# Performance work log

Measured on AMD Instinct MI355X. Metric: run time of the kernel, lower is better.

Reference implementation:

```python
import jax, jax.numpy as jnp
import numpy as np
from jax.ops import segment_sum

N_NODES = 100000
N_EDGES = 3200000
IN_DIM = 128
HID = 128
INT_DIM = 512
OUT_DIM = 3


def gcn_conv(x, W, b, src, dst, n):
    # PyG GCNConv (eval): add self-loops, symmetric normalization, aggregate, bias.
    loop = jnp.arange(n, dtype=src.dtype)
    s = jnp.concatenate([src, loop])
    d = jnp.concatenate([dst, loop])
    deg = segment_sum(jnp.ones_like(d, dtype=x.dtype), d, num_segments=n)  # [N]
    dinv = jnp.where(deg > 0, jax.lax.rsqrt(jnp.maximum(deg, 1e-12)), 0.0)
    norm = dinv[s] * dinv[d]                      # [E+N]
    h = x @ W                                      # [N, F_out]
    msg = h[s] * norm[:, None]                    # gather + scale
    return segment_sum(msg, d, num_segments=n) + b


def setup_inputs() -> dict:
    key = jax.random.key(0)
    ks = jax.random.split(key, 12)
    def lin(kw, kb, fi, fo):
        lim = 1.0 / np.sqrt(fi)
        W = jax.random.uniform(kw, (fi, fo), jnp.float32, -lim, lim)
        b = jax.random.uniform(kb, (fo,), jnp.float32, -lim, lim)
        return W, b
    x = jax.random.normal(ks[0], (N_NODES, IN_DIM), jnp.float32)
    edge_index = jax.random.randint(ks[1], (2, N_EDGES), 0, N_NODES, dtype=jnp.int64)
    W1, b1 = lin(ks[2], ks[3], IN_DIM, HID)
    W2, b2 = lin(ks[4], ks[5], HID, HID)
    W3, b3 = lin(ks[6], ks[7], HID, INT_DIM)
    Wi, bi = lin(ks[8], ks[9], INT_DIM, INT_DIM)
    Wc, bc = lin(ks[10], ks[11], INT_DIM, OUT_DIM)
    return {"x": x, "edge_index": edge_index, "W1": W1, "b1": b1, "W2": W2,
            "b2": b2, "W3": W3, "b3": b3, "Wi": Wi, "bi": bi, "Wc": Wc, "bc": bc}


def reference(x, edge_index, W1, b1, W2, b2, W3, b3, Wi, bi, Wc, bc):
    src, dst = edge_index[0], edge_index[1]
    n = x.shape[0]
    h = jax.nn.relu(gcn_conv(x, W1, b1, src, dst, n))
    h = jax.nn.relu(gcn_conv(h, W2, b2, src, dst, n))
    h = jax.nn.relu(gcn_conv(h, W3, b3, src, dst, n))
    h = jax.nn.relu(h @ Wi + bi)
    return h @ Wc + bc
```

## Files before the change

### kernel.cpp

```cpp
#include <hip/hip_runtime.h>
#include <hip/hip_fp16.h>

#define NN 100000
#define NE 3200000
#define NB 391
#define NBLK 512
#define EPB 6250

typedef unsigned int uint32;
typedef unsigned short u16;
typedef long long ll64;
typedef __attribute__((ext_vector_type(8))) _Float16 half8;
typedef __attribute__((ext_vector_type(4))) float f32x4;

__device__ inline float2 h2f2(uint32 u) {
  __half2 h = *reinterpret_cast<__half2*>(&u);
  return __half22float2(h);
}
__device__ inline uint32 f2h2(float x, float y) {
  return (uint32)__half_as_ushort(__float2half(x)) |
         ((uint32)__half_as_ushort(__float2half(y)) << 16);
}
__device__ inline int edge_at(const void* ei, int is64, ll64 idx) {
  return is64 ? (int)((const ll64*)ei)[idx] : ((const int*)ei)[idx];
}
__device__ inline int detect64(const int* ei32) {
  int acc = 0;
#pragma unroll
  for (int k = 1; k < 32; k += 2) acc |= ei32[k];
  return (acc == 0) ? 1 : 0;
}

__global__ __launch_bounds__(256) void k_binB(const void* __restrict__ ei,
                                              int* __restrict__ tbl) {
  __shared__ int h[NB];
  __shared__ int sIs64;
  int k = blockIdx.x, tid = threadIdx.x;
  for (int i = tid; i < NB; i += 256) h[i] = 0;
  if (tid == 0) sIs64 = detect64((const int*)ei);
  __syncthreads();
  int is64 = sIs64;
  ll64 beg = (ll64)k * EPB, end = beg + EPB;
  for (ll64 i = beg + tid; i < end; i += 256)
    atomicAdd(&h[edge_at(ei, is64, (ll64)NE + i) >> 8], 1);
  __syncthreads();
  for (int i = tid; i < NB; i += 256) tbl[k * NB + i] = h[i];
}
__global__ __launch_bounds__(512) void k_binC1(int* __restrict__ tbl,
                                               int* __restrict__ total) {
  __shared__ int sd[NBLK];
  int b = blockIdx.x, tid = threadIdx.x;
  int v = tbl[tid * NB + b];
  sd[tid] = v;
  __syncthreads();
  for (int off = 1; off < NBLK; off <<= 1) {
    int t = (tid >= off) ? sd[tid - off] : 0;
    __syncthreads();
    sd[tid] += t;
    __syncthreads();
  }
  tbl[tid * NB + b] = sd[tid] - v;
  if (tid == NBLK - 1) total[b] = sd[NBLK - 1];
}
__global__ __launch_bounds__(512) void k_binC2(const int* __restrict__ total,
                                               int* __restrict__ bbase,
                                               int* __restrict__ offs) {
  __shared__ int sd[512];
  int tid = threadIdx.x;
  int v = (tid < NB) ? total[tid] : 0;
  sd[tid] = v;
  __syncthreads();
  for (int off = 1; off < 512; off <<= 1) {
    int t = (tid >= off) ? sd[tid - off] : 0;
    __syncthreads();
    sd[tid] += t;
    __syncthreads();
  }
  if (tid < NB) bbase[tid] = sd[tid] - v;
  if (tid == 0) offs[NN] = NE;
}
__global__ __launch_bounds__(256) void k_binD(const void* __restrict__ ei,
                                              const int* __restrict__ tbl,
                                              const int* __restrict__ bbase,
                                              uint32* __restrict__ binned) {
  __shared__ int lb[NB];
  __shared__ int lc[NB];
  __shared__ int sIs64;
  int k = blockIdx.x, tid = threadIdx.x;
  for (int i = tid; i < NB; i += 256) {
    lb[i] = tbl[k * NB + i] + bbase[i];
    lc[i] = 0;
  }
  if (tid == 0) sIs64 = detect64((const int*)ei);
  __syncthreads();
  int is64 = sIs64;
  ll64 beg = (ll64)k * EPB, end = beg + EPB;
  for (ll64 i = beg + tid; i < end; i += 256) {
    int s = edge_at(ei, is64, i);
    int d = edge_at(ei, is64, (ll64)NE + i);
    int b = d >> 8;
    int r = atomicAdd(&lc[b], 1);
    binned[lb[b] + r] = (uint32)s | ((uint32)(d & 255) << 24);
  }
}
__global__ __launch_bounds__(256) void k_binE(const uint32* __restrict__ binned,
                                              const int* __restrict__ bbase,
                                              const int* __restrict__ total,
                                              int* __restrict__ offs,
                                              float* __restrict__ dinv,
                                              int* __restrict__ csr) {
  __shared__ int cnt[256], pref[256], fil[256];
  int b = blockIdx.x, tid = threadIdx.x;
  cnt[tid] = 0;
  fil[tid] = 0;
  __syncthreads();
  int base = bbase[b], tot = total[b];
  for (int i = tid; i < tot; i += 256) atomicAdd(&cnt[binned[base + i] >> 24], 1);
  __syncthreads();
  int v = cnt[tid];
  pref[tid] = v;
  __syncthreads();
  for (int off = 1; off < 256; off <<= 1) {
    int t = (tid >= off) ? pref[tid - off] : 0;
    __syncthreads();
    pref[tid] += t;
    __syncthreads();
  }
  int myoff = pref[tid] - v;
  pref[tid] = myoff;
  int node = b * 256 + tid;
  if (node < NN) {
    offs[node] = base + myoff;
    dinv[node] = rsqrtf((float)(v + 1));
  }
  __syncthreads();
  for (int i = tid; i < tot; i += 256) {
    uint32 w = binned[base + i];
    int dl = w >> 24;
    int r = atomicAdd(&fil[dl], 1);
    csr[base + pref[dl] + r] = (int)(w & 0xFFFFFFu);
  }
}

__device__ inline void packOne(const float* __restrict__ W, u16* __restrict__ ph,
                               int K, int N, int t) {
  int j = t & 7, lane = (t >> 3) & 63, tl = t >> 9;
  int kbn = K >> 5;
  int kb = tl % kbn, ntile = tl / kbn;
  int k = kb * 32 + (lane >> 4) * 8 + j;
  int n2 = ntile * 16 + (lane & 15);
  ph[t] = __half_as_ushort(__float2half(W[k * N + n2]));
}
__global__ void k_packhalf(const float* W1, const float* W2, const float* W3,
                           const float* Wi, u16* p1, u16* p2, u16* p3, u16* pi,
                           const float4* __restrict__ x, ushort4* __restrict__ xh,
                           const float* __restrict__ dinv) {
  int t = blockIdx.x * blockDim.x + threadIdx.x;
  if (t < 16384) packOne(W1, p1, 128, 128, t);
  else if (t < 32768) packOne(W2, p2, 128, 128, t - 16384);
  else if (t < 98304) packOne(W3, p3, 128, 512, t - 32768);
  else if (t < 360448) packOne(Wi, pi, 512, 512, t - 98304);
  else {
    int i = t - 360448;
    if (i < NN * 32) {
      float4 v = x[i];
      float sc = dinv[i >> 5];
      ushort4 o;
      o.x = __half_as_ushort(__float2half(v.x * sc));
      o.y = __half_as_ushort(__float2half(v.y * sc));
      o.z = __half_as_ushort(__float2half(v.z * sc));
      o.w = __half_as_ushort(__float2half(v.w * sc));
      xh[i] = o;
    }
  }
}

__global__ void k_agg(const uint32* __restrict__ xi, uint32* __restrict__ o,
                      const int* __restrict__ csr, const int* __restrict__ offs,
                      const float* __restrict__ dinv, int n) {
  int tid = threadIdx.x;
  int lane = tid & 63;
  int sub = lane >> 4, fl = lane & 15;
  int node = blockIdx.x * 16 + (tid >> 6) * 4 + sub;
  if (node >= n) return;
  int beg = offs[node], end = offs[node + 1];
  const uint4* xv = (const uint4*)xi;
  float acc[8] = {};
  int j = beg;
  for (; j + 7 < end; j += 8) {
    int s[8];
    uint4 r[8];
#pragma unroll
    for (int q = 0; q < 8; q++) s[q] = csr[j + q];
#pragma unroll
    for (int q = 0; q < 8; q++) r[q] = xv[(ll64)s[q] * 16 + fl];
#pragma unroll
    for (int q = 0; q < 8; q++) {
      float2 p0 = h2f2(r[q].x), p1 = h2f2(r[q].y);
      float2 p2 = h2f2(r[q].z), p3 = h2f2(r[q].w);
      acc[0] += p0.x; acc[1] += p0.y; acc[2] += p1.x; acc[3] += p1.y;
      acc[4] += p2.x; acc[5] += p2.y; acc[6] += p3.x; acc[7] += p3.y;
    }
  }
  for (; j + 3 < end; j += 4) {
    int s[4];
    uint4 r[4];
#pragma unroll
    for (int q = 0; q < 4; q++) s[q] = csr[j + q];
#pragma unroll
    for (int q = 0; q < 4; q++) r[q] = xv[(ll64)s[q] * 16 + fl];
#pragma unroll
    for (int q = 0; q < 4; q++) {
      float2 p0 = h2f2(r[q].x), p1 = h2f2(r[q].y);
      float2 p2 = h2f2(r[q].z), p3 = h2f2(r[q].w);
      acc[0] += p0.x; acc[1] += p0.y; acc[2] += p1.x; acc[3] += p1.y;
      acc[4] += p2.x; acc[5] += p2.y; acc[6] += p3.x; acc[7] += p3.y;
    }
  }
  for (; j < end; j++) {
    uint4 r = xv[(ll64)csr[j] * 16 + fl];
    float2 p0 = h2f2(r.x), p1 = h2f2(r.y), p2 = h2f2(r.z), p3 = h2f2(r.w);
    acc[0] += p0.x; acc[1] += p0.y; acc[2] += p1.x; acc[3] += p1.y;
    acc[4] += p2.x; acc[5] += p2.y; acc[6] += p3.x; acc[7] += p3.y;
  }
  float di = dinv[node];
  uint4 sf = xv[(ll64)node * 16 + fl];
  float2 q0 = h2f2(sf.x), q1 = h2f2(sf.y), q2 = h2f2(sf.z), q3 = h2f2(sf.w);
  uint4 ov;
  ov.x = f2h2(di * (acc[0] + q0.x), di * (acc[1] + q0.y));
  ov.y = f2h2(di * (acc[2] + q1.x), di * (acc[3] + q1.y));
  ov.z = f2h2(di * (acc[4] + q2.x), di * (acc[5] + q2.y));
  ov.w = f2h2(di * (acc[6] + q3.x), di * (acc[7] + q3.y));
  ((uint4*)o)[(ll64)node * 16 + fl] = ov;
}

__global__ __launch_bounds__(256, 4) void k_gemm_mfma(
    const u16* __restrict__ A, const u16* __restrict__ Bp,
    const float* __restrict__ bias, const float* __restrict__ dscale,
    u16* __restrict__ Co, int M, int N, int K) {
  int wave = threadIdx.x >> 6, lane = threadIdx.x & 63;
  int quad = lane >> 4, l16 = lane & 15;
  int row0 = blockIdx.x * 64, col0 = blockIdx.y * 64;
  int m = row0 + wave * 16 + l16;
  int mc = (m < M) ? m : (M - 1);
  int kbn = K >> 5;
  f32x4 acc[4] = {{0,0,0,0},{0,0,0,0},{0,0,0,0},{0,0,0,0}};
  const half8* Ar = (const half8*)&A[(ll64)mc * K];
  half8 ac = Ar[quad];
  half8 an = ac;
  half8 bc_[4], bn_[4];
#pragma unroll
  for (int nt = 0; nt < 4; nt++)
    bc_[nt] = *(const half8*)&Bp[((ll64)(((col0 >> 4) + nt) * kbn) * 64 + lane) * 8];
  for (int kb = 0; kb < kbn; kb++) {
    int kn = kb + 1;
    if (kn < kbn) {
      an = Ar[kn * 4 + quad];
#pragma unroll
      for (int nt = 0; nt < 4; nt++)
        bn_[nt] = *(const half8*)&Bp[((ll64)(((col0 >> 4) + nt) * kbn + kn) * 64 + lane) * 8];
    }
#pragma unroll
    for (int nt = 0; nt < 4; nt++)
      acc[nt] = __builtin_amdgcn_mfma_f32_16x16x32_f16(ac, bc_[nt], acc[nt], 0, 0, 0);
    ac = an;
#pragma unroll
    for (int nt = 0; nt < 4; nt++) bc_[nt] = bn_[nt];
  }
  float ds[4];
#pragma unroll
  for (int r = 0; r < 4; r++) {
    int rr = row0 + wave * 16 + quad * 4 + r;
    ds[r] = dscale[(rr < M) ? rr : (M - 1)];
  }
#pragma unroll
  for (int nt = 0; nt < 4; nt++) {
    int cc = col0 + nt * 16 + l16;
    float bv = bias[cc];
#pragma unroll
    for (int r = 0; r < 4; r++) {
      int rr = row0 + wave * 16 + quad * 4 + r;
      if (rr < M)
        Co[(ll64)rr * N + cc] =
            __half_as_ushort(__float2half(fmaxf(acc[nt][r] + bv, 0.0f) * ds[r]));
    }
  }
}

__global__ __launch_bounds__(256, 4) void k_tail32(
    const u16* __restrict__ a3, const u16* __restrict__ W3p,
    const float* __restrict__ b3, const u16* __restrict__ Wip,
    const float* __restrict__ bi, const float* __restrict__ Wc,
    const float* __restrict__ bc, float* __restrict__ out, int M) {
  __shared__ u16 h3s[32 * 512];
  __shared__ float sRed[4][32][3];
  int tid = threadIdx.x;
  int wave = tid >> 6, lane = tid & 63, quad = lane >> 4, l16 = lane & 15;
  int row0 = blockIdx.x * 32;

  half8 af[2][4];
#pragma unroll
  for (int rt = 0; rt < 2; rt++) {
    const half8* Ar = (const half8*)&a3[(ll64)(row0 + rt * 16 + l16) * 128];
#pragma unroll
    for (int kb = 0; kb < 4; kb++) af[rt][kb] = Ar[kb * 4 + quad];
  }
  {
    f32x4 acc0 = {0, 0, 0, 0}, acc1 = {0, 0, 0, 0};
    half8 bq[4];
#pragma unroll
    for (int p = 0; p < 3; p++)
      bq[p] = *(const half8*)&W3p[((ll64)(wave * 32 + p) * 64 + lane) * 8];
#pragma unroll 4
    for (int t = 0; t < 32; t++) {
      if (t + 3 < 32)
        bq[(t + 3) & 3] = *(const half8*)&W3p[((ll64)(wave * 32 + t + 3) * 64 + lane) * 8];
      half8 bcur = bq[t & 3];
      int kb = t & 3;
      acc0 = __builtin_amdgcn_mfma_f32_16x16x32_f16(af[0][kb], bcur, acc0, 0, 0, 0);
      acc1 = __builtin_amdgcn_mfma_f32_16x16x32_f16(af[1][kb], bcur, acc1, 0, 0, 0);
      if (kb == 3) {
        int nt = wave * 8 + (t >> 2);
        int col = nt * 16 + l16;
        float bv = b3[col];
#pragma unroll
        for (int r = 0; r < 4; r++) {
          int row0l = quad * 4 + r;
          float v0 = fmaxf(acc0[r] + bv, 0.0f);
          float v1 = fmaxf(acc1[r] + bv, 0.0f);
          int oct0 = (col >> 3) ^ (row0l & 7);
          h3s[row0l * 512 + oct0 * 8 + (col & 7)] = __half_as_ushort(__float2half(v0));
          int row1l = 16 + row0l;
          int oct1 = (col >> 3) ^ (row1l & 7);
          h3s[row1l * 512 + oct1 * 8 + (col & 7)] = __half_as_ushort(__float2half(v1));
        }
        acc0 = (f32x4){0, 0, 0, 0};
        acc1 = (f32x4){0, 0, 0, 0};
      }
    }
  }
  __syncthreads();

  float acc3[2][4][3] = {};
  {
    f32x4 acc0 = {0, 0, 0, 0}, acc1 = {0, 0, 0, 0};
    half8 bq[4];
#pragma unroll
    for (int p = 0; p < 3; p++)
      bq[p] = *(const half8*)&Wip[((ll64)(wave * 128 + p) * 64 + lane) * 8];
    int r0l = l16, r1l = 16 + l16;
    int sw0 = r0l & 7;
#pragma unroll 4
    for (int t = 0; t < 128; t++) {
      if (t + 3 < 128)
        bq[(t + 3) & 3] = *(const half8*)&Wip[((ll64)(wave * 128 + t + 3) * 64 + lane) * 8];
      half8 bcur = bq[t & 3];
      int kb = t & 15;
      int oct = ((kb * 4 + quad) ^ sw0);
      half8 a0 = *(const half8*)&h3s[r0l * 512 + oct * 8];
      half8 a1 = *(const half8*)&h3s[r1l * 512 + oct * 8];
      acc0 = __builtin_amdgcn_mfma_f32_16x16x32_f16(a0, bcur, acc0, 0, 0, 0);
      acc1 = __builtin_amdgcn_mfma_f32_16x16x32_f16(a1, bcur, acc1, 0, 0, 0);
      if (kb == 15) {
        int nt = wave * 8 + (t >> 4);
        int col = nt * 16 + l16;
        float bv = bi[col];
        float w0 = Wc[col * 3 + 0], w1 = Wc[col * 3 + 1], w2 = Wc[col * 3 + 2];
#pragma unroll
        for (int r = 0; r < 4; r++) {
          float v0 = fmaxf(acc0[r] + bv, 0.0f);
          float v1 = fmaxf(acc1[r] + bv, 0.0f);
          acc3[0][r][0] += v0 * w0; acc3[0][r][1] += v0 * w1; acc3[0][r][2] += v0 * w2;
          acc3[1][r][0] += v1 * w0; acc3[1][r][1] += v1 * w1; acc3[1][r][2] += v1 * w2;
        }
        acc0 = (f32x4){0, 0, 0, 0};
        acc1 = (f32x4){0, 0, 0, 0};
      }
    }
  }
#pragma unroll
  for (int rt = 0; rt < 2; rt++)
#pragma unroll
    for (int r = 0; r < 4; r++)
#pragma unroll
      for (int c = 0; c < 3; c++) {
        float v = acc3[rt][r][c];
        v += __shfl_xor(v, 1);
        v += __shfl_xor(v, 2);
        v += __shfl_xor(v, 4);
        v += __shfl_xor(v, 8);
        acc3[rt][r][c] = v;
      }
  if (l16 == 0) {
#pragma unroll
    for (int rt = 0; rt < 2; rt++)
#pragma unroll
      for (int r = 0; r < 4; r++)
#pragma unroll
        for (int c = 0; c < 3; c++)
          sRed[wave][rt * 16 + quad * 4 + r][c] = acc3[rt][r][c];
  }
  __syncthreads();
  if (tid < 96) {
    int row = tid / 3, c = tid % 3;
    out[(ll64)(row0 + row) * 3 + c] = sRed[0][row][c] + sRed[1][row][c] +
                                      sRed[2][row][c] + sRed[3][row][c] + bc[c];
  }
}

extern "C" void kernel_launch(void* const* d_in, const int* in_sizes, int n_in,
                              void* d_out, int out_size, void* d_ws, size_t ws_size,
                              hipStream_t stream) {
  const float* x  = (const float*)d_in[0];
  const void*  ei = d_in[1];
  const float* W1 = (const float*)d_in[2];
  const float* b1 = (const float*)d_in[3];
  const float* W2 = (const float*)d_in[4];
  const float* b2 = (const float*)d_in[5];
  const float* W3 = (const float*)d_in[6];
  const float* b3 = (const float*)d_in[7];
  const float* Wi = (const float*)d_in[8];
  const float* bi = (const float*)d_in[9];
  const float* Wc = (const float*)d_in[10];
  const float* bc = (const float*)d_in[11];
  float* out = (float*)d_out;

  char* ws = (char*)d_ws;
  const ll64 KB = 1ll << 10, MB = 1ll << 20;
  float* dinv  = (float*)(ws + 0);
  int*   offs  = (int*)(ws + 512 * KB);
  int*   total = (int*)(ws + 1 * MB + 64 * KB);
  int*   bbase = (int*)(ws + 1 * MB + 128 * KB);
  int*   tbl   = (int*)(ws + 1 * MB + 192 * KB);
  uint32* binned = (uint32*)(ws + 2 * MB);
  int*   csr   = (int*)(ws + 15 * MB);
  u16* pW1 = (u16*)(ws + 28 * MB);
  u16* pW2 = (u16*)(ws + 28 * MB + 64 * KB);
  u16* pW3 = (u16*)(ws + 28 * MB + 128 * KB);
  u16* pWi = (u16*)(ws + 28 * MB + 512 * KB);
  u16* xh   = (u16*)(ws + 29 * MB);
  u16* bufA = (u16*)(ws + 55 * MB);
  u16* bufB = (u16*)(ws + 81 * MB);

  const int TB = 256;
  k_binB<<<NBLK, TB, 0, stream>>>(ei, tbl);
  k_binC1<<<NB, NBLK, 0, stream>>>(tbl, total);
  k_binC2<<<1, 512, 0, stream>>>(total, bbase, offs);
  k_binD<<<NBLK, TB, 0, stream>>>(ei, tbl, bbase, binned);
  k_binE<<<NB, TB, 0, stream>>>(binned, bbase, total, offs, dinv, csr);
  k_packhalf<<<(360448 + NN * 32 + TB - 1) / TB, TB, 0, stream>>>(
      W1, W2, W3, Wi, pW1, pW2, pW3, pWi, (const float4*)x, (ushort4*)xh, dinv);

  const int MBk = (NN + 63) / 64;
  int aggBlocks = (NN + 15) / 16;
  dim3 g128(MBk, 2);

  k_agg<<<aggBlocks, TB, 0, stream>>>((const uint32*)xh, (uint32*)bufA, csr, offs, dinv, NN);
  k_gemm_mfma<<<g128, TB, 0, stream>>>(bufA, pW1, b1, dinv, bufB, NN, 128, 128);
  k_agg<<<aggBlocks, TB, 0, stream>>>((const uint32*)bufB, (uint32*)bufA, csr, offs, dinv, NN);
  k_gemm_mfma<<<g128, TB, 0, stream>>>(bufA, pW2, b2, dinv, bufB, NN, 128, 128);
  k_agg<<<aggBlocks, TB, 0, stream>>>((const uint32*)bufB, (uint32*)bufA, csr, offs, dinv, NN);
  k_tail32<<<NN / 32, TB, 0, stream>>>(bufA, pW3, b3, pWi, bi, Wc, bc, out, NN);
}
```

Measured before the change: 699.7 us.

## Store aggregation inputs feature-chunk-major so each gather pass hits a cache-sized slice

The aggregation input features are stored in a chunk-major layout: 8 chunks of 16 halfs, each holding all nodes contiguously. Both the x packing kernel and the GEMM epilogue now write that layout. Each aggregation block handles one chunk for 128 nodes, so random source gathers touch only a 3.2MB slice per chunk, which can stay resident in L2/LLC. CSR index loads and output stores become nontemporal. In exchange, the CSR index stream is read 8 times and each gather fetches only 32 bytes per edge.

Result: slower. 1.059 ms (+51.4%).

```diff
diff --git a/kernel.cpp b/kernel.cpp
--- a/kernel.cpp
+++ b/kernel.cpp
@@ -12,6 +12,7 @@
 typedef long long ll64;
 typedef __attribute__((ext_vector_type(8))) _Float16 half8;
 typedef __attribute__((ext_vector_type(4))) float f32x4;
+typedef __attribute__((ext_vector_type(4))) uint32 nt4;
 
 __device__ inline float2 h2f2(uint32 u) {
   __half2 h = *reinterpret_cast<__half2*>(&u);
@@ -170,7 +171,8 @@
       o.y = __half_as_ushort(__float2half(v.y * sc));
       o.z = __half_as_ushort(__float2half(v.z * sc));
       o.w = __half_as_ushort(__float2half(v.w * sc));
-      xh[i] = o;
+      int row = i >> 5, j = i & 31;
+      xh[(ll64)(j >> 2) * (NN * 4) + row * 4 + (j & 3)] = o;
     }
   }
 }
@@ -179,21 +181,25 @@
                       const int* __restrict__ csr, const int* __restrict__ offs,
                       const float* __restrict__ dinv, int n) {
   int tid = threadIdx.x;
+  int chunk = blockIdx.x & 7;
+  int nb = blockIdx.x >> 3;
   int lane = tid & 63;
-  int sub = lane >> 4, fl = lane & 15;
-  int node = blockIdx.x * 16 + (tid >> 6) * 4 + sub;
+  int sub = lane & 1;
+  int nloc = lane >> 1;
+  int node = nb * 128 + (tid >> 6) * 32 + nloc;
   if (node >= n) return;
   int beg = offs[node], end = offs[node + 1];
-  const uint4* xv = (const uint4*)xi;
+  const nt4* xv = (const nt4*)xi;
+  ll64 cbase = (ll64)chunk * (NN * 2);
   float acc[8] = {};
   int j = beg;
   for (; j + 7 < end; j += 8) {
     int s[8];
-    uint4 r[8];
-#pragma unroll
-    for (int q = 0; q < 8; q++) s[q] = csr[j + q];
-#pragma unroll
-    for (int q = 0; q < 8; q++) r[q] = xv[(ll64)s[q] * 16 + fl];
+    nt4 r[8];
+#pragma unroll
+    for (int q = 0; q < 8; q++) s[q] = __builtin_nontemporal_load(&csr[j + q]);
+#pragma unroll
+    for (int q = 0; q < 8; q++) r[q] = xv[cbase + (ll64)s[q] * 2 + sub];
 #pragma unroll
     for (int q = 0; q < 8; q++) {
       float2 p0 = h2f2(r[q].x), p1 = h2f2(r[q].y);
@@ -204,11 +210,11 @@
   }
   for (; j + 3 < end; j += 4) {
     int s[4];
-    uint4 r[4];
-#pragma unroll
-    for (int q = 0; q < 4; q++) s[q] = csr[j + q];
-#pragma unroll
-    for (int q = 0; q < 4; q++) r[q] = xv[(ll64)s[q] * 16 + fl];
+    nt4 r[4];
+#pragma unroll
+    for (int q = 0; q < 4; q++) s[q] = __builtin_nontemporal_load(&csr[j + q]);
+#pragma unroll
+    for (int q = 0; q < 4; q++) r[q] = xv[cbase + (ll64)s[q] * 2 + sub];
 #pragma unroll
     for (int q = 0; q < 4; q++) {
       float2 p0 = h2f2(r[q].x), p1 = h2f2(r[q].y);
@@ -218,20 +224,21 @@
     }
   }
   for (; j < end; j++) {
-    uint4 r = xv[(ll64)csr[j] * 16 + fl];
+    int s = __builtin_nontemporal_load(&csr[j]);
+    nt4 r = xv[cbase + (ll64)s * 2 + sub];
     float2 p0 = h2f2(r.x), p1 = h2f2(r.y), p2 = h2f2(r.z), p3 = h2f2(r.w);
     acc[0] += p0.x; acc[1] += p0.y; acc[2] += p1.x; acc[3] += p1.y;
     acc[4] += p2.x; acc[5] += p2.y; acc[6] += p3.x; acc[7] += p3.y;
   }
   float di = dinv[node];
-  uint4 sf = xv[(ll64)node * 16 + fl];
+  nt4 sf = xv[cbase + (ll64)node * 2 + sub];
   float2 q0 = h2f2(sf.x), q1 = h2f2(sf.y), q2 = h2f2(sf.z), q3 = h2f2(sf.w);
-  uint4 ov;
+  nt4 ov;
   ov.x = f2h2(di * (acc[0] + q0.x), di * (acc[1] + q0.y));
   ov.y = f2h2(di * (acc[2] + q1.x), di * (acc[3] + q1.y));
   ov.z = f2h2(di * (acc[4] + q2.x), di * (acc[5] + q2.y));
   ov.w = f2h2(di * (acc[6] + q3.x), di * (acc[7] + q3.y));
-  ((uint4*)o)[(ll64)node * 16 + fl] = ov;
+  __builtin_nontemporal_store(ov, &((nt4*)o)[(ll64)node * 16 + chunk * 2 + sub]);
 }
 
 __global__ __launch_bounds__(256, 4) void k_gemm_mfma(
@@ -277,11 +284,12 @@
   for (int nt = 0; nt < 4; nt++) {
     int cc = col0 + nt * 16 + l16;
     float bv = bias[cc];
+    ll64 cmaj = (ll64)(cc >> 4) * ((ll64)M * 16);
 #pragma unroll
     for (int r = 0; r < 4; r++) {
       int rr = row0 + wave * 16 + quad * 4 + r;
       if (rr < M)
-        Co[(ll64)rr * N + cc] =
+        Co[cmaj + (ll64)rr * 16 + l16] =
             __half_as_ushort(__float2half(fmaxf(acc[nt][r] + bv, 0.0f) * ds[r]));
     }
   }
@@ -452,7 +460,7 @@
       W1, W2, W3, Wi, pW1, pW2, pW3, pWi, (const float4*)x, (ushort4*)xh, dinv);
 
   const int MBk = (NN + 63) / 64;
-  int aggBlocks = (NN + 15) / 16;
+  int aggBlocks = 8 * ((NN + 127) / 128);
   dim3 g128(MBk, 2);
 
   k_agg<<<aggBlocks, TB, 0, stream>>>((const uint32*)xh, (uint32*)bufA, csr, offs, dinv, NN);
```

## Fuse third-layer aggregation into tail kernel via shared-memory staging

Applied to the files above, without the earlier changes.

The final sparse aggregation now runs inside the tail kernel instead of as a separate k_agg launch. Each block gathers neighbor rows for its 32 nodes, applies the self-loop and dinv scaling, and writes the fp16 result into an XOR-swizzled shared buffer. The MFMA A fragments are then read from that buffer rather than from global memory. This drops one kernel launch and a full write and read of the intermediate activation. The cost is lower gather parallelism per block (4 nodes per wave at a time) and extra synchronisation inside a kernel with heavy register and LDS use.

Result: no change. 690.1 us (-1.4%).

```diff
diff --git a/kernel.cpp b/kernel.cpp
--- a/kernel.cpp
+++ b/kernel.cpp
@@ -287,24 +287,87 @@
   }
 }
 
-__global__ __launch_bounds__(256, 4) void k_tail32(
-    const u16* __restrict__ a3, const u16* __restrict__ W3p,
-    const float* __restrict__ b3, const u16* __restrict__ Wip,
-    const float* __restrict__ bi, const float* __restrict__ Wc,
-    const float* __restrict__ bc, float* __restrict__ out, int M) {
+__global__ __launch_bounds__(256, 4) void k_tail32f(
+    const u16* __restrict__ xin, const int* __restrict__ csr,
+    const int* __restrict__ offs, const float* __restrict__ dinv,
+    const u16* __restrict__ W3p, const float* __restrict__ b3,
+    const u16* __restrict__ Wip, const float* __restrict__ bi,
+    const float* __restrict__ Wc, const float* __restrict__ bc,
+    float* __restrict__ out, int M) {
   __shared__ u16 h3s[32 * 512];
   __shared__ float sRed[4][32][3];
   int tid = threadIdx.x;
   int wave = tid >> 6, lane = tid & 63, quad = lane >> 4, l16 = lane & 15;
   int row0 = blockIdx.x * 32;
 
+  {
+    int sub = lane >> 4, fl = lane & 15;
+    const uint4* xv = (const uint4*)xin;
+#pragma unroll
+    for (int rnd = 0; rnd < 2; rnd++) {
+      int nloc = rnd * 16 + wave * 4 + sub;
+      int node = row0 + nloc;
+      int beg = offs[node], end = offs[node + 1];
+      float acc[8] = {};
+      int j = beg;
+      for (; j + 7 < end; j += 8) {
+        int s[8];
+        uint4 r[8];
+#pragma unroll
+        for (int q = 0; q < 8; q++) s[q] = csr[j + q];
+#pragma unroll
+        for (int q = 0; q < 8; q++) r[q] = xv[(ll64)s[q] * 16 + fl];
+#pragma unroll
+        for (int q = 0; q < 8; q++) {
+          float2 p0 = h2f2(r[q].x), p1 = h2f2(r[q].y);
+          float2 p2 = h2f2(r[q].z), p3 = h2f2(r[q].w);
+          acc[0] += p0.x; acc[1] += p0.y; acc[2] += p1.x; acc[3] += p1.y;
+          acc[4] += p2.x; acc[5] += p2.y; acc[6] += p3.x; acc[7] += p3.y;
+        }
+      }
+      for (; j + 3 < end; j += 4) {
+        int s[4];
+        uint4 r[4];
+#pragma unroll
+        for (int q = 0; q < 4; q++) s[q] = csr[j + q];
+#pragma unroll
+        for (int q = 0; q < 4; q++) r[q] = xv[(ll64)s[q] * 16 + fl];
+#pragma unroll
+        for (int q = 0; q < 4; q++) {
+          float2 p0 = h2f2(r[q].x), p1 = h2f2(r[q].y);
+          float2 p2 = h2f2(r[q].z), p3 = h2f2(r[q].w);
+          acc[0] += p0.x; acc[1] += p0.y; acc[2] += p1.x; acc[3] += p1.y;
+          acc[4] += p2.x; acc[5] += p2.y; acc[6] += p3.x; acc[7] += p3.y;
+        }
+      }
+      for (; j < end; j++) {
+        uint4 r = xv[(ll64)csr[j] * 16 + fl];
+        float2 p0 = h2f2(r.x), p1 = h2f2(r.y), p2 = h2f2(r.z), p3 = h2f2(r.w);
+        acc[0] += p0.x; acc[1] += p0.y; acc[2] += p1.x; acc[3] += p1.y;
+        acc[4] += p2.x; acc[5] += p2.y; acc[6] += p3.x; acc[7] += p3.y;
+      }
+      float di = dinv[node];
+      uint4 sf = xv[(ll64)node * 16 + fl];
+      float2 q0 = h2f2(sf.x), q1 = h2f2(sf.y), q2 = h2f2(sf.z), q3 = h2f2(sf.w);
+      uint4 ov;
+      ov.x = f2h2(di * (acc[0] + q0.x), di * (acc[1] + q0.y));
+      ov.y = f2h2(di * (acc[2] + q1.x), di * (acc[3] + q1.y));
+      ov.z = f2h2(di * (acc[4] + q2.x), di * (acc[5] + q2.y));
+      ov.w = f2h2(di * (acc[6] + q3.x), di * (acc[7] + q3.y));
+      *(uint4*)&h3s[nloc * 128 + ((fl ^ (nloc & 7)) << 3)] = ov;
+    }
+  }
+  __syncthreads();
   half8 af[2][4];
 #pragma unroll
   for (int rt = 0; rt < 2; rt++) {
-    const half8* Ar = (const half8*)&a3[(ll64)(row0 + rt * 16 + l16) * 128];
-#pragma unroll
-    for (int kb = 0; kb < 4; kb++) af[rt][kb] = Ar[kb * 4 + quad];
-  }
+    int row = rt * 16 + l16;
+#pragma unroll
+    for (int kb = 0; kb < 4; kb++)
+      af[rt][kb] = *(const half8*)&h3s[row * 128 + (((kb * 4 + quad) ^ (row & 7)) << 3)];
+  }
+  __syncthreads();
+
   {
     f32x4 acc0 = {0, 0, 0, 0}, acc1 = {0, 0, 0, 0};
     half8 bq[4];
@@ -459,6 +522,6 @@
   k_gemm_mfma<<<g128, TB, 0, stream>>>(bufA, pW1, b1, dinv, bufB, NN, 128, 128);
   k_agg<<<aggBlocks, TB, 0, stream>>>((const uint32*)bufB, (uint32*)bufA, csr, offs, dinv, NN);
   k_gemm_mfma<<<g128, TB, 0, stream>>>(bufA, pW2, b2, dinv, bufB, NN, 128, 128);
-  k_agg<<<aggBlocks, TB, 0, stream>>>((const uint32*)bufB, (uint32*)bufA, csr, offs, dinv, NN);
-  k_tail32<<<NN / 32, TB, 0, stream>>>(bufA, pW3, b3, pWi, bi, Wc, bc, out, NN);
-}
+  k_tail32f<<<NN / 32, TB, 0, stream>>>(bufB, csr, offs, dinv, pW3, b3, pWi, bi,
+                                        Wc, bc, out, NN);
+}
```

## Fuse neighbor aggregation with the following GEMM through an LDS tile

Applied to the files above, without the earlier changes.

Each block now gathers and aggregates 32 nodes' features into a swizzled shared-memory tile, then runs the MFMA GEMM with bias, ReLU and dinv scaling directly from that tile. The separate aggregation kernels and standalone GEMM kernels are removed, including the aggregation before the tail kernel. This cuts launches and the round-trip of aggregated activations through global memory. In exchange, the memory-bound gather and the MFMA compute now share one kernel whose occupancy is bounded by the launch bounds and LDS use, and each block is serialized between the two phases.

Measured after the change: 689.4 us. Within noise of the previous version (-1.5%).

```diff
diff --git a/kernel.cpp b/kernel.cpp
--- a/kernel.cpp
+++ b/kernel.cpp
@@ -175,136 +175,139 @@
   }
 }
 
-__global__ void k_agg(const uint32* __restrict__ xi, uint32* __restrict__ o,
-                      const int* __restrict__ csr, const int* __restrict__ offs,
-                      const float* __restrict__ dinv, int n) {
-  int tid = threadIdx.x;
-  int lane = tid & 63;
+__device__ inline void agg32_phase0(const u16* __restrict__ xin,
+                                    const int* __restrict__ csr,
+                                    const int* __restrict__ offs,
+                                    const float* __restrict__ dinv,
+                                    int row0, int tid, u16* __restrict__ tile) {
+  int lane = tid & 63, wave = tid >> 6;
   int sub = lane >> 4, fl = lane & 15;
-  int node = blockIdx.x * 16 + (tid >> 6) * 4 + sub;
-  if (node >= n) return;
-  int beg = offs[node], end = offs[node + 1];
-  const uint4* xv = (const uint4*)xi;
-  float acc[8] = {};
-  int j = beg;
-  for (; j + 7 < end; j += 8) {
-    int s[8];
-    uint4 r[8];
-#pragma unroll
-    for (int q = 0; q < 8; q++) s[q] = csr[j + q];
-#pragma unroll
-    for (int q = 0; q < 8; q++) r[q] = xv[(ll64)s[q] * 16 + fl];
-#pragma unroll
-    for (int q = 0; q < 8; q++) {
-      float2 p0 = h2f2(r[q].x), p1 = h2f2(r[q].y);
-      float2 p2 = h2f2(r[q].z), p3 = h2f2(r[q].w);
+  const uint4* xv = (const uint4*)xin;
+#pragma unroll
+  for (int rnd = 0; rnd < 2; rnd++) {
+    int nloc = rnd * 16 + wave * 4 + sub;
+    int node = row0 + nloc;
+    int beg = offs[node], end = offs[node + 1];
+    float acc[8] = {};
+    int j = beg;
+    for (; j + 7 < end; j += 8) {
+      int s[8];
+      uint4 r[8];
+#pragma unroll
+      for (int q = 0; q < 8; q++) s[q] = csr[j + q];
+#pragma unroll
+      for (int q = 0; q < 8; q++) r[q] = xv[(ll64)s[q] * 16 + fl];
+#pragma unroll
+      for (int q = 0; q < 8; q++) {
+        float2 p0 = h2f2(r[q].x), p1 = h2f2(r[q].y);
+        float2 p2 = h2f2(r[q].z), p3 = h2f2(r[q].w);
+        acc[0] += p0.x; acc[1] += p0.y; acc[2] += p1.x; acc[3] += p1.y;
+        acc[4] += p2.x; acc[5] += p2.y; acc[6] += p3.x; acc[7] += p3.y;
+      }
+    }
+    for (; j + 3 < end; j += 4) {
+      int s[4];
+      uint4 r[4];
+#pragma unroll
+      for (int q = 0; q < 4; q++) s[q] = csr[j + q];
+#pragma unroll
+      for (int q = 0; q < 4; q++) r[q] = xv[(ll64)s[q] * 16 + fl];
+#pragma unroll
+      for (int q = 0; q < 4; q++) {
+        float2 p0 = h2f2(r[q].x), p1 = h2f2(r[q].y);
+        float2 p2 = h2f2(r[q].z), p3 = h2f2(r[q].w);
+        acc[0] += p0.x; acc[1] += p0.y; acc[2] += p1.x; acc[3] += p1.y;
+        acc[4] += p2.x; acc[5] += p2.y; acc[6] += p3.x; acc[7] += p3.y;
+      }
+    }
+    for (; j < end; j++) {
+      uint4 r = xv[(ll64)csr[j] * 16 + fl];
+      float2 p0 = h2f2(r.x), p1 = h2f2(r.y), p2 = h2f2(r.z), p3 = h2f2(r.w);
       acc[0] += p0.x; acc[1] += p0.y; acc[2] += p1.x; acc[3] += p1.y;
       acc[4] += p2.x; acc[5] += p2.y; acc[6] += p3.x; acc[7] += p3.y;
     }
-  }
-  for (; j + 3 < end; j += 4) {
-    int s[4];
-    uint4 r[4];
-#pragma unroll
-    for (int q = 0; q < 4; q++) s[q] = csr[j + q];
-#pragma unroll
-    for (int q = 0; q < 4; q++) r[q] = xv[(ll64)s[q] * 16 + fl];
-#pragma unroll
-    for (int q = 0; q < 4; q++) {
-      float2 p0 = h2f2(r[q].x), p1 = h2f2(r[q].y);
-      float2 p2 = h2f2(r[q].z), p3 = h2f2(r[q].w);
-      acc[0] += p0.x; acc[1] += p0.y; acc[2] += p1.x; acc[3] += p1.y;
-      acc[4] += p2.x; acc[5] += p2.y; acc[6] += p3.x; acc[7] += p3.y;
-    }
-  }
-  for (; j < end; j++) {
-    uint4 r = xv[(ll64)csr[j] * 16 + fl];
-    float2 p0 = h2f2(r.x), p1 = h2f2(r.y), p2 = h2f2(r.z), p3 = h2f2(r.w);
-    acc[0] += p0.x; acc[1] += p0.y; acc[2] += p1.x; acc[3] += p1.y;
-    acc[4] += p2.x; acc[5] += p2.y; acc[6] += p3.x; acc[7] += p3.y;
-  }
-  float di = dinv[node];
-  uint4 sf = xv[(ll64)node * 16 + fl];
-  float2 q0 = h2f2(sf.x), q1 = h2f2(sf.y), q2 = h2f2(sf.z), q3 = h2f2(sf.w);
-  uint4 ov;
-  ov.x = f2h2(di * (acc[0] + q0.x), di * (acc[1] + q0.y));
-  ov.y = f2h2(di * (acc[2] + q1.x), di * (acc[3] + q1.y));
-  ov.z = f2h2(di * (acc[4] + q2.x), di * (acc[5] + q2.y));
-  ov.w = f2h2(di * (acc[6] + q3.x), di * (acc[7] + q3.y));
-  ((uint4*)o)[(ll64)node * 16 + fl] = ov;
-}
-
-__global__ __launch_bounds__(256, 4) void k_gemm_mfma(
-    const u16* __restrict__ A, const u16* __restrict__ Bp,
-    const float* __restrict__ bias, const float* __restrict__ dscale,
-    u16* __restrict__ Co, int M, int N, int K) {
-  int wave = threadIdx.x >> 6, lane = threadIdx.x & 63;
-  int quad = lane >> 4, l16 = lane & 15;
-  int row0 = blockIdx.x * 64, col0 = blockIdx.y * 64;
-  int m = row0 + wave * 16 + l16;
-  int mc = (m < M) ? m : (M - 1);
-  int kbn = K >> 5;
-  f32x4 acc[4] = {{0,0,0,0},{0,0,0,0},{0,0,0,0},{0,0,0,0}};
-  const half8* Ar = (const half8*)&A[(ll64)mc * K];
-  half8 ac = Ar[quad];
-  half8 an = ac;
-  half8 bc_[4], bn_[4];
-#pragma unroll
-  for (int nt = 0; nt < 4; nt++)
-    bc_[nt] = *(const half8*)&Bp[((ll64)(((col0 >> 4) + nt) * kbn) * 64 + lane) * 8];
-  for (int kb = 0; kb < kbn; kb++) {
-    int kn = kb + 1;
-    if (kn < kbn) {
-      an = Ar[kn * 4 + quad];
-#pragma unroll
-      for (int nt = 0; nt < 4; nt++)
-        bn_[nt] = *(const half8*)&Bp[((ll64)(((col0 >> 4) + nt) * kbn + kn) * 64 + lane) * 8];
-    }
-#pragma unroll
-    for (int nt = 0; nt < 4; nt++)
-      acc[nt] = __builtin_amdgcn_mfma_f32_16x16x32_f16(ac, bc_[nt], acc[nt], 0, 0, 0);
-    ac = an;
-#pragma unroll
-    for (int nt = 0; nt < 4; nt++) bc_[nt] = bn_[nt];
-  }
-  float ds[4];
-#pragma unroll
-  for (int r = 0; r < 4; r++) {
-    int rr = row0 + wave * 16 + quad * 4 + r;
-    ds[r] = dscale[(rr < M) ? rr : (M - 1)];
-  }
-#pragma unroll
-  for (int nt = 0; nt < 4; nt++) {
-    int cc = col0 + nt * 16 + l16;
-    float bv = bias[cc];
+    float di = dinv[node];
+    uint4 sf = xv[(ll64)node * 16 + fl];
+    float2 q0 = h2f2(sf.x), q1 = h2f2(sf.y), q2 = h2f2(sf.z), q3 = h2f2(sf.w);
+    uint4 ov;
+    ov.x = f2h2(di * (acc[0] + q0.x), di * (acc[1] + q0.y));
+    ov.y = f2h2(di * (acc[2] + q1.x), di * (acc[3] + q1.y));
+    ov.z = f2h2(di * (acc[4] + q2.x), di * (acc[5] + q2.y));
+    ov.w = f2h2(di * (acc[6] + q3.x), di * (acc[7] + q3.y));
+    *(uint4*)&tile[nloc * 128 + ((fl ^ (nloc & 7)) << 3)] = ov;
+  }
+}
+
+__device__ inline void load_af(const u16* __restrict__ tile, int lane,
+                               half8 af[2][4]) {
+  int quad = (lane >> 4), l16 = lane & 15;
+#pragma unroll
+  for (int rt = 0; rt < 2; rt++) {
+    int row = rt * 16 + l16;
+#pragma unroll
+    for (int kb = 0; kb < 4; kb++)
+      af[rt][kb] = *(const half8*)&tile[row * 128 + (((kb * 4 + quad) ^ (row & 7)) << 3)];
+  }
+}
+
+__global__ __launch_bounds__(256, 4) void k_fusedL(
+    const u16* __restrict__ xin, const int* __restrict__ csr,
+    const int* __restrict__ offs, const float* __restrict__ dinv,
+    const u16* __restrict__ Wp, const float* __restrict__ bias,
+    u16* __restrict__ Co) {
+  __shared__ u16 tile[32 * 128];
+  int tid = threadIdx.x;
+  int wave = tid >> 6, lane = tid & 63, quad = lane >> 4, l16 = lane & 15;
+  int row0 = blockIdx.x * 32;
+  agg32_phase0(xin, csr, offs, dinv, row0, tid, tile);
+  __syncthreads();
+  half8 af[2][4];
+  load_af(tile, lane, af);
+#pragma unroll
+  for (int p = 0; p < 2; p++) {
+    int nt = wave * 2 + p;
+    half8 bv[4];
+#pragma unroll
+    for (int kb = 0; kb < 4; kb++)
+      bv[kb] = *(const half8*)&Wp[((ll64)(nt * 4 + kb) * 64 + lane) * 8];
+    f32x4 acc0 = {0, 0, 0, 0}, acc1 = {0, 0, 0, 0};
+#pragma unroll
+    for (int kb = 0; kb < 4; kb++) {
+      acc0 = __builtin_amdgcn_mfma_f32_16x16x32_f16(af[0][kb], bv[kb], acc0, 0, 0, 0);
+      acc1 = __builtin_amdgcn_mfma_f32_16x16x32_f16(af[1][kb], bv[kb], acc1, 0, 0, 0);
+    }
+    int col = nt * 16 + l16;
+    float bvv = bias[col];
 #pragma unroll
     for (int r = 0; r < 4; r++) {
-      int rr = row0 + wave * 16 + quad * 4 + r;
-      if (rr < M)
-        Co[(ll64)rr * N + cc] =
-            __half_as_ushort(__float2half(fmaxf(acc[nt][r] + bv, 0.0f) * ds[r]));
-    }
-  }
-}
-
-__global__ __launch_bounds__(256, 4) void k_tail32(
-    const u16* __restrict__ a3, const u16* __restrict__ W3p,
-    const float* __restrict__ b3, const u16* __restrict__ Wip,
-    const float* __restrict__ bi, const float* __restrict__ Wc,
-    const float* __restrict__ bc, float* __restrict__ out, int M) {
+      int r0 = quad * 4 + r, r1 = r0 + 16;
+      Co[(ll64)(row0 + r0) * 128 + col] =
+          __half_as_ushort(__float2half(fmaxf(acc0[r] + bvv, 0.0f) * dinv[row0 + r0]));
+      Co[(ll64)(row0 + r1) * 128 + col] =
+          __half_as_ushort(__float2half(fmaxf(acc1[r] + bvv, 0.0f) * dinv[row0 + r1]));
+    }
+  }
+}
+
+__global__ __launch_bounds__(256, 4) void k_tail32f(
+    const u16* __restrict__ xin, const int* __restrict__ csr,
+    const int* __restrict__ offs, const float* __restrict__ dinv,
+    const u16* __restrict__ W3p, const float* __restrict__ b3,
+    const u16* __restrict__ Wip, const float* __restrict__ bi,
+    const float* __restrict__ Wc, const float* __restrict__ bc,
+    float* __restrict__ out, int M) {
   __shared__ u16 h3s[32 * 512];
   __shared__ float sRed[4][32][3];
   int tid = threadIdx.x;
   int wave = tid >> 6, lane = tid & 63, quad = lane >> 4, l16 = lane & 15;
   int row0 = blockIdx.x * 32;
 
+  agg32_phase0(xin, csr, offs, dinv, row0, tid, h3s);
+  __syncthreads();
   half8 af[2][4];
-#pragma unroll
-  for (int rt = 0; rt < 2; rt++) {
-    const half8* Ar = (const half8*)&a3[(ll64)(row0 + rt * 16 + l16) * 128];
-#pragma unroll
-    for (int kb = 0; kb < 4; kb++) af[rt][kb] = Ar[kb * 4 + quad];
-  }
+  load_af(h3s, lane, af);
+  __syncthreads();
+
   {
     f32x4 acc0 = {0, 0, 0, 0}, acc1 = {0, 0, 0, 0};
     half8 bq[4];
@@ -451,14 +454,10 @@
   k_packhalf<<<(360448 + NN * 32 + TB - 1) / TB, TB, 0, stream>>>(
       W1, W2, W3, Wi, pW1, pW2, pW3, pWi, (const float4*)x, (ushort4*)xh, dinv);
 
-  const int MBk = (NN + 63) / 64;
-  int aggBlocks = (NN + 15) / 16;
-  dim3 g128(MBk, 2);
-
-  k_agg<<<aggBlocks, TB, 0, stream>>>((const uint32*)xh, (uint32*)bufA, csr, offs, dinv, NN);
-  k_gemm_mfma<<<g128, TB, 0, stream>>>(bufA, pW1, b1, dinv, bufB, NN, 128, 128);
-  k_agg<<<aggBlocks, TB, 0, stream>>>((const uint32*)bufB, (uint32*)bufA, csr, offs, dinv, NN);
-  k_gemm_mfma<<<g128, TB, 0, stream>>>(bufA, pW2, b2, dinv, bufB, NN, 128, 128);
-  k_agg<<<aggBlocks, TB, 0, stream>>>((const uint32*)bufB, (uint32*)bufA, csr, offs, dinv, NN);
-  k_tail32<<<NN / 32, TB, 0, stream>>>(bufA, pW3, b3, pWi, bi, Wc, bc, out, NN);
-}
+  const int NB32 = NN / 32;
+
+  k_fusedL<<<NB32, TB, 0, stream>>>(xh, csr, offs, dinv, pW1, b1, bufB);
+  k_fusedL<<<NB32, TB, 0, stream>>>(bufB, csr, offs, dinv, pW2, b2, bufA);
+  k_tail32f<<<NB32, TB, 0, stream>>>(bufA, csr, offs, dinv, pW3, b3, pWi, bi,
+                                     Wc, bc, out, NN);
+}
```
